# Kernel tuning notes

Measured on AMD Instinct MI355X. Metric: run time of the kernel, lower is better.

The kernel has to match this reference:

```python
import jax, jax.numpy as jnp
import numpy as np

N_NODES = 50000
N_EDGES = 800000
IN_DIM = 128
FEAT = 64
HID = 64
OUT = 64
EA_DIM = 3  # edge_attr columns; concat -> weight in_dim = 3*channels


def _uniform(key, shape, lo=-1.0, hi=1.0):
    return jax.random.uniform(key, shape, jnp.float32, lo, hi)


def setup_inputs() -> dict:
    key = jax.random.key(0)
    ks = jax.random.split(key, 12)
    x = jax.random.normal(ks[0], (N_NODES, IN_DIM), jnp.float32)
    edge_index = jax.random.randint(ks[1], (2, N_EDGES), 0, N_NODES, jnp.int32)
    edge_attr = jax.random.uniform(ks[2], (N_EDGES, EA_DIM), jnp.float32)
    # linear_pre (nn.Linear default init approximated; values irrelevant for correctness)
    pre_w = _uniform(ks[3], (IN_DIM, FEAT), -0.08, 0.08)
    pre_b = _uniform(ks[4], (FEAT,), -0.08, 0.08)
    # SAGEConvEGNN weights: uniform(-1, 1), shape [3*in, out]
    w1 = _uniform(ks[5], (EA_DIM * FEAT, HID))
    b1 = _uniform(ks[6], (HID,))
    w2 = _uniform(ks[7], (EA_DIM * HID, HID))
    b2 = _uniform(ks[8], (HID,))
    w3 = _uniform(ks[9], (EA_DIM * HID, OUT))
    b3 = _uniform(ks[10], (OUT,))
    return {"x": x, "edge_index": edge_index, "edge_attr": edge_attr,
            "pre_w": pre_w, "pre_b": pre_b,
            "w1": w1, "b1": b1, "w2": w2, "b2": b2, "w3": w3, "b3": b3}


def _sage_conv(h, src, tgt, edge_attr, w, b, n_nodes):
    # message: x_j scaled by each of the 3 edge_attr columns, concatenated -> [E, 3*C]
    xj = h[src]                                              # gather [E, C]
    msg = (edge_attr[:, :, None] * xj[:, None, :]).reshape(xj.shape[0], -1)
    s = jax.ops.segment_sum(msg, tgt, num_segments=n_nodes)  # scatter-sum [N, 3C]
    cnt = jax.ops.segment_sum(jnp.ones((src.shape[0],), msg.dtype), tgt,
                              num_segments=n_nodes)
    agg = s / jnp.maximum(cnt, 1.0)[:, None]                 # mean; 0 for isolated nodes
    return agg @ w + b


def reference(x, edge_index, edge_attr, pre_w, pre_b, w1, b1, w2, b2, w3, b3):
    src, tgt = edge_index[0], edge_index[1]  # message from j=src aggregated at i=tgt
    n = x.shape[0]
    h = x @ pre_w + pre_b                     # linear_pre
    h = jax.nn.relu(_sage_conv(h, src, tgt, edge_attr, w1, b1, n))
    h = jax.nn.relu(_sage_conv(h, src, tgt, edge_attr, w2, b2, n))
    h = _sage_conv(h, src, tgt, edge_attr, w3, b3, n)
    # F.normalize(p=2, dim=-1) with eps=1e-12
    norm = jnp.sqrt(jnp.sum(h * h, axis=-1, keepdims=True))
    return h / jnp.maximum(norm, 1e-12)
```

## Files before the change

kernel.cpp:

```cpp
#include <hip/hip_runtime.h>
#include <hip/hip_bf16.h>

#define NN 50000
#define NE 800000
#define IND 128
#define C 64
#define NBUCK 196

typedef __hip_bfloat16 bf16;
typedef __attribute__((ext_vector_type(8))) short s8v;
typedef __attribute__((ext_vector_type(4))) float f4v;

__device__ __forceinline__ float to_f(float v) { return v; }
__device__ __forceinline__ float to_f(bf16 v)  { return __bfloat162float(v); }

__device__ __forceinline__ unsigned short f2b(float v) {
    unsigned u = __float_as_uint(v);
    return (unsigned short)((u + 0x7FFFu + ((u >> 16) & 1u)) >> 16);
}
__device__ __forceinline__ float b2f(unsigned short u) {
    return __uint_as_float((unsigned)u << 16);
}

__global__ void detect_kernel(const unsigned* __restrict__ xu, int* __restrict__ flag,
                              int* __restrict__ zbase) {
    int lane = threadIdx.x;
    for (int i = lane; i < 512; i += 64) zbase[i] = 0;
    unsigned u  = xu[lane];
    unsigned ex = (u >> 7) & 0xFF;
    int vote = (ex >= 90 && ex <= 144) ? 1 : 0;
#pragma unroll
    for (int off = 32; off; off >>= 1) vote += __shfl_xor(vote, off, 64);
    if (lane == 0) { flag[0] = (vote < 40) ? 1 : 0; flag[1] = 0; }
}

__global__ __launch_bounds__(256) void prep_kernel(const void* pw, const void* w0,
        const void* w1, const void* w2, int* __restrict__ flagp,
        const int* __restrict__ tgt,
        unsigned short* __restrict__ oh, unsigned short* __restrict__ ol,
        int* __restrict__ bcnt, int* __restrict__ boff, int* __restrict__ off) {
    __shared__ int lc[NBUCK];
    __shared__ int rank_s;
    __shared__ int wsum[4];
    int blk = blockIdx.x;
    int tid = threadIdx.x;
    if (blk < 176) {
        int gid = blk * 256 + tid;
        const void* w; int nT, idx, base;
        if (gid < 8192) { w = pw; nT = 4; idx = gid; base = 0; }
        else {
            int r = gid - 8192; int l = r / 12288; idx = r % 12288; nT = 6;
            w = (l == 0) ? w0 : (l == 1) ? w1 : w2; base = 8192 + l * 12288;
        }
        int j = idx & 7, lane = (idx >> 3) & 63, r2 = idx >> 9;
        int t = r2 % nT, ct = r2 / nT;
        int k = 32 * t + ((lane >> 4) << 3) + j;
        int col = 16 * ct + (lane & 15);
        if (*flagp) {
            float v = ((const float*)w)[k * 64 + col];
            unsigned short hi = f2b(v);
            oh[base + idx] = hi;
            ol[base + idx] = f2b(v - b2f(hi));
        } else {
            oh[base + idx] = ((const unsigned short*)w)[k * 64 + col];
        }
        return;
    }
    for (int i = tid; i < NBUCK; i += 256) lc[i] = 0;
    __syncthreads();
    int e0 = (blk - 176) * 2048;
#pragma unroll
    for (int k = 0; k < 8; ++k) {
        int e = e0 + (k << 8) + tid;
        if (e < NE) atomicAdd(&lc[tgt[e] >> 8], 1);
    }
    __syncthreads();
    for (int i = tid; i < NBUCK; i += 256) if (lc[i]) atomicAdd(&bcnt[i], lc[i]);
    __syncthreads();
    if (tid == 0) {
        __threadfence();
        rank_s = atomicAdd(&flagp[1], 1);
    }
    __syncthreads();
    int nCnt = (int)gridDim.x - 176;
    if (rank_s == nCnt - 1) {
        int lane = tid & 63, wv = tid >> 6;
        int v = (tid < NBUCK) ? atomicAdd(&bcnt[tid], 0) : 0;
        int incl = v;
#pragma unroll
        for (int d = 1; d < 64; d <<= 1) { int t = __shfl_up(incl, d, 64); if (lane >= d) incl += t; }
        if (lane == 63) wsum[wv] = incl;
        __syncthreads();
        int wbase = 0;
#pragma unroll
        for (int j = 0; j < 4; ++j) wbase += (j < wv) ? wsum[j] : 0;
        if (tid < NBUCK) boff[tid] = wbase + incl - v;
        if (tid == 0) { boff[NBUCK] = NE; off[NN] = NE; }
    }
}

template <typename T>
__device__ __forceinline__ void binA_impl(int* lcnt, int* lbase,
                                          const int* __restrict__ src,
                                          const int* __restrict__ tgt,
                                          const T* __restrict__ ea,
                                          const int* __restrict__ boff,
                                          int* __restrict__ ccur,
                                          float4* __restrict__ stg) {
    int tid = threadIdx.x;
    for (int i = tid; i < NBUCK; i += 256) lcnt[i] = 0;
    __syncthreads();
    int e0 = blockIdx.x * 2048;
    float ex[8], ey[8], ez[8];
    unsigned ew[8];
    int eb[8], er[8];
#pragma unroll
    for (int k = 0; k < 8; ++k) {
        int e = e0 + (k << 8) + tid;
        if (e < NE) {
            int t = tgt[e];
            int s = src[e];
            eb[k] = t >> 8;
            ew[k] = ((unsigned)t << 16) | (unsigned)s;
            ex[k] = to_f(ea[e * 3 + 0]);
            ey[k] = to_f(ea[e * 3 + 1]);
            ez[k] = to_f(ea[e * 3 + 2]);
            er[k] = atomicAdd(&lcnt[eb[k]], 1);
        } else eb[k] = -1;
    }
    __syncthreads();
    for (int i = tid; i < NBUCK; i += 256) {
        int c = lcnt[i];
        int g = c ? atomicAdd(&ccur[i], c) : 0;
        lbase[i] = boff[i] + g;
    }
    __syncthreads();
#pragma unroll
    for (int k = 0; k < 8; ++k) {
        if (eb[k] >= 0) {
            float4 r;
            r.x = ex[k]; r.y = ey[k]; r.z = ez[k];
            r.w = __uint_as_float(ew[k]);
            stg[lbase[eb[k]] + er[k]] = r;
        }
    }
}

__global__ __launch_bounds__(256) void binA_kernel(const int* __restrict__ src,
                                                   const int* __restrict__ tgt,
                                                   const void* ea,
                                                   const int* __restrict__ boff,
                                                   const int* __restrict__ flagp,
                                                   int* __restrict__ ccur,
                                                   float4* __restrict__ stg) {
    __shared__ int lcnt[NBUCK];
    __shared__ int lbase[NBUCK];
    if (*flagp) binA_impl<float>(lcnt, lbase, src, tgt, (const float*)ea, boff, ccur, stg);
    else        binA_impl<bf16>(lcnt, lbase, src, tgt, (const bf16*)ea, boff, ccur, stg);
}

template <typename T>
__device__ __forceinline__ void preM_body(int nb, const T* __restrict__ x,
                                          const unsigned short* __restrict__ wfh,
                                          const unsigned short* __restrict__ wfl,
                                          const T* __restrict__ b,
                                          unsigned short* __restrict__ h) {
    int tid = threadIdx.x;
    int lane = tid & 63, wv = tid >> 6;
    int m = lane & 15, g = lane >> 4;
    int arow = nb + wv * 16 + m;
    bool okrow = arow < NN;
    f4v acc[4] = {};
    for (int t = 0; t < 4; ++t) {
        if constexpr (sizeof(T) == 4) {
            float av[8];
            if (okrow) {
                const float* xr = (const float*)x + (size_t)arow * IND + t * 32 + g * 8;
                float4 v0 = *(const float4*)xr;
                float4 v1 = *(const float4*)(xr + 4);
                av[0] = v0.x; av[1] = v0.y; av[2] = v0.z; av[3] = v0.w;
                av[4] = v1.x; av[5] = v1.y; av[6] = v1.z; av[7] = v1.w;
            } else {
#pragma unroll
                for (int j = 0; j < 8; ++j) av[j] = 0.f;
            }
            s8v ahi, alo;
#pragma unroll
            for (int j = 0; j < 8; ++j) {
                unsigned short hi = f2b(av[j]);
                ahi[j] = (short)hi;
                alo[j] = (short)f2b(av[j] - b2f(hi));
            }
#pragma unroll
            for (int ct = 0; ct < 4; ++ct) {
                int fo = ((ct * 4 + t) * 64 + lane) * 8;
                s8v bh = *(const s8v*)&wfh[fo];
                s8v bl = *(const s8v*)&wfl[fo];
                acc[ct] = __builtin_amdgcn_mfma_f32_16x16x32_bf16(ahi, bh, acc[ct], 0, 0, 0);
                acc[ct] = __builtin_amdgcn_mfma_f32_16x16x32_bf16(alo, bh, acc[ct], 0, 0, 0);
                acc[ct] = __builtin_amdgcn_mfma_f32_16x16x32_bf16(ahi, bl, acc[ct], 0, 0, 0);
            }
        } else {
            s8v ahi = {};
            if (okrow)
                ahi = *(const s8v*)((const unsigned short*)x + (size_t)arow * IND + t * 32 + g * 8);
#pragma unroll
            for (int ct = 0; ct < 4; ++ct) {
                int fo = ((ct * 4 + t) * 64 + lane) * 8;
                s8v bh = *(const s8v*)&wfh[fo];
                acc[ct] = __builtin_amdgcn_mfma_f32_16x16x32_bf16(ahi, bh, acc[ct], 0, 0, 0);
            }
        }
    }
#pragma unroll
    for (int r = 0; r < 4; ++r) {
        int drow = nb + wv * 16 + g * 4 + r;
        if (drow < NN) {
#pragma unroll
            for (int ct = 0; ct < 4; ++ct)
                h[(size_t)drow * C + 16 * ct + m] = f2b(acc[ct][r] + to_f(b[16 * ct + m]));
        }
    }
}

__global__ __launch_bounds__(256) void binB_pre_kernel(const float4* __restrict__ stg,
        const int* __restrict__ boff, int* __restrict__ off, float4* __restrict__ edge,
        const void* x, const unsigned short* __restrict__ wfh,
        const unsigned short* __restrict__ wfl, const void* pb,
        const int* __restrict__ flagp, unsigned short* __restrict__ h) {
    __shared__ int lcnt[256];
    __shared__ int lexcl[256];
    __shared__ int lfill[256];
    __shared__ int wsum[4];
    int tid = threadIdx.x;
    if (blockIdx.x < NBUCK) {
        int b = blockIdx.x;
        int n0 = b << 8;
        int cb = boff[b], ce = boff[b + 1];
        lcnt[tid] = 0;
        __syncthreads();
        for (int i = cb + tid; i < ce; i += 256) {
            unsigned w = __float_as_uint(stg[i].w);
            atomicAdd(&lcnt[(w >> 16) & 255], 1);
        }
        __syncthreads();
        int lane = tid & 63, wv = tid >> 6;
        int v = lcnt[tid];
        int incl = v;
#pragma unroll
        for (int d = 1; d < 64; d <<= 1) { int t = __shfl_up(incl, d, 64); if (lane >= d) incl += t; }
        if (lane == 63) wsum[wv] = incl;
        __syncthreads();
        int wbase = 0;
#pragma unroll
        for (int j = 0; j < 4; ++j) wbase += (j < wv) ? wsum[j] : 0;
        lexcl[tid] = wbase + incl - v;
        lfill[tid] = 0;
        __syncthreads();
        int n = n0 + tid;
        if (n <= NN) off[n] = cb + lexcl[tid];
        for (int i = cb + tid; i < ce; i += 256) {
            float4 r = stg[i];
            unsigned w = __float_as_uint(r.w);
            int l = (int)(w >> 16) & 255;
            int rk = atomicAdd(&lfill[l], 1);
            r.w = __uint_as_float(w & 0xFFFFu);
            edge[cb + lexcl[l] + rk] = r;
        }
    } else {
        int nb = (blockIdx.x - NBUCK) * 64;
        if (*flagp) preM_body<float>(nb, (const float*)x, wfh, wfl, (const float*)pb, h);
        else        preM_body<bf16>(nb, (const bf16*)x, wfh, wfl, (const bf16*)pb, h);
    }
}

__global__ __launch_bounds__(256) void agg_kernel(const unsigned short* __restrict__ hb,
                                                  const float4* __restrict__ edge,
                                                  const int* __restrict__ off,
                                                  unsigned short* __restrict__ sh,
                                                  unsigned short* __restrict__ sl) {
    int f = threadIdx.x & 63;
    int n = blockIdx.x * 4 + (threadIdx.x >> 6);
    int beg = __builtin_amdgcn_readfirstlane(off[n]);
    int end = __builtin_amdgcn_readfirstlane(off[n + 1]);
    float a0 = 0.f, a1 = 0.f, a2 = 0.f;
    int cnt = end - beg;
    int m4 = beg + (cnt & ~3);
    int e = beg;
    if (beg + 8 <= m4) {
        float4 c0 = edge[e],     c1 = edge[e + 1], c2 = edge[e + 2], c3 = edge[e + 3];
        float4 d0 = edge[e + 4], d1 = edge[e + 5], d2 = edge[e + 6], d3 = edge[e + 7];
        float h0 = b2f(hb[(__float_as_int(c0.w) << 6) + f]);
        float h1 = b2f(hb[(__float_as_int(c1.w) << 6) + f]);
        float h2 = b2f(hb[(__float_as_int(c2.w) << 6) + f]);
        float h3 = b2f(hb[(__float_as_int(c3.w) << 6) + f]);
        int e2 = beg + 8;
        while (e2 < m4) {
            float g0 = b2f(hb[(__float_as_int(d0.w) << 6) + f]);
            float g1 = b2f(hb[(__float_as_int(d1.w) << 6) + f]);
            float g2 = b2f(hb[(__float_as_int(d2.w) << 6) + f]);
            float g3 = b2f(hb[(__float_as_int(d3.w) << 6) + f]);
            float4 n0 = edge[e2], n1 = edge[e2 + 1], n2 = edge[e2 + 2], n3 = edge[e2 + 3];
            a0 += c0.x * h0; a1 += c0.y * h0; a2 += c0.z * h0;
            a0 += c1.x * h1; a1 += c1.y * h1; a2 += c1.z * h1;
            a0 += c2.x * h2; a1 += c2.y * h2; a2 += c2.z * h2;
            a0 += c3.x * h3; a1 += c3.y * h3; a2 += c3.z * h3;
            c0 = d0; c1 = d1; c2 = d2; c3 = d3;
            h0 = g0; h1 = g1; h2 = g2; h3 = g3;
            d0 = n0; d1 = n1; d2 = n2; d3 = n3;
            e2 += 4;
        }
        float g0 = b2f(hb[(__float_as_int(d0.w) << 6) + f]);
        float g1 = b2f(hb[(__float_as_int(d1.w) << 6) + f]);
        float g2 = b2f(hb[(__float_as_int(d2.w) << 6) + f]);
        float g3 = b2f(hb[(__float_as_int(d3.w) << 6) + f]);
        a0 += c0.x * h0; a1 += c0.y * h0; a2 += c0.z * h0;
        a0 += c1.x * h1; a1 += c1.y * h1; a2 += c1.z * h1;
        a0 += c2.x * h2; a1 += c2.y * h2; a2 += c2.z * h2;
        a0 += c3.x * h3; a1 += c3.y * h3; a2 += c3.z * h3;
        a0 += d0.x * g0; a1 += d0.y * g0; a2 += d0.z * g0;
        a0 += d1.x * g1; a1 += d1.y * g1; a2 += d1.z * g1;
        a0 += d2.x * g2; a1 += d2.y * g2; a2 += d2.z * g2;
        a0 += d3.x * g3; a1 += d3.y * g3; a2 += d3.z * g3;
        e = m4;
    } else if (beg + 4 <= m4) {
        float4 c0 = edge[e], c1 = edge[e + 1], c2 = edge[e + 2], c3 = edge[e + 3];
        float h0 = b2f(hb[(__float_as_int(c0.w) << 6) + f]);
        float h1 = b2f(hb[(__float_as_int(c1.w) << 6) + f]);
        float h2 = b2f(hb[(__float_as_int(c2.w) << 6) + f]);
        float h3 = b2f(hb[(__float_as_int(c3.w) << 6) + f]);
        a0 += c0.x * h0; a1 += c0.y * h0; a2 += c0.z * h0;
        a0 += c1.x * h1; a1 += c1.y * h1; a2 += c1.z * h1;
        a0 += c2.x * h2; a1 += c2.y * h2; a2 += c2.z * h2;
        a0 += c3.x * h3; a1 += c3.y * h3; a2 += c3.z * h3;
        e = m4;
    }
    for (; e < end; ++e) {
        float4 r = edge[e];
        float hv = b2f(hb[(__float_as_int(r.w) << 6) + f]);
        a0 += r.x * hv; a1 += r.y * hv; a2 += r.z * hv;
    }
    float iv = 1.0f / fmaxf((float)cnt, 1.0f);
    size_t base = (size_t)n * 192;
    float v0 = a0 * iv, v1 = a1 * iv, v2 = a2 * iv;
    unsigned short x0 = f2b(v0), x1 = f2b(v1), x2 = f2b(v2);
    sh[base + f]       = x0; sl[base + f]       = f2b(v0 - b2f(x0));
    sh[base + 64 + f]  = x1; sl[base + 64 + f]  = f2b(v1 - b2f(x1));
    sh[base + 128 + f] = x2; sl[base + 128 + f] = f2b(v2 - b2f(x2));
}

template <typename T, int MODE>
__device__ __forceinline__ void gemmM_impl(const unsigned short* __restrict__ sh,
                                           const unsigned short* __restrict__ sl,
                                           const unsigned short* __restrict__ wfh,
                                           const unsigned short* __restrict__ wfl,
                                           const T* __restrict__ b,
                                           unsigned short* __restrict__ hout, T* __restrict__ out) {
    int tid = threadIdx.x;
    int nb  = blockIdx.x * 64;
    int lane = tid & 63, wv = tid >> 6;
    int m = lane & 15, g = lane >> 4;
    int arow = nb + wv * 16 + m;
    bool okrow = arow < NN;
    const unsigned short* shrow = sh + (size_t)arow * 192 + g * 8;
    const unsigned short* slrow = sl + (size_t)arow * 192 + g * 8;
    f4v acc[4] = {};
    for (int t = 0; t < 6; ++t) {
        s8v ahi = {}, alo = {};
        if (okrow) {
            ahi = *(const s8v*)(shrow + t * 32);
            alo = *(const s8v*)(slrow + t * 32);
        }
#pragma unroll
        for (int ct = 0; ct < 4; ++ct) {
            int fo = ((ct * 6 + t) * 64 + lane) * 8;
            s8v bh = *(const s8v*)&wfh[fo];
            acc[ct] = __builtin_amdgcn_mfma_f32_16x16x32_bf16(ahi, bh, acc[ct], 0, 0, 0);
            acc[ct] = __builtin_amdgcn_mfma_f32_16x16x32_bf16(alo, bh, acc[ct], 0, 0, 0);
            if constexpr (sizeof(T) == 4) {
                s8v bl = *(const s8v*)&wfl[fo];
                acc[ct] = __builtin_amdgcn_mfma_f32_16x16x32_bf16(ahi, bl, acc[ct], 0, 0, 0);
            }
        }
    }
    float vv[4][4];
#pragma unroll
    for (int ct = 0; ct < 4; ++ct) {
        float bv = to_f(b[16 * ct + m]);
#pragma unroll
        for (int r = 0; r < 4; ++r) vv[ct][r] = acc[ct][r] + bv;
    }
    if constexpr (MODE == 0) {
#pragma unroll
        for (int r = 0; r < 4; ++r) {
            int drow = nb + wv * 16 + g * 4 + r;
            if (drow < NN) {
#pragma unroll
                for (int ct = 0; ct < 4; ++ct)
                    hout[(size_t)drow * C + 16 * ct + m] = f2b(fmaxf(vv[ct][r], 0.f));
            }
        }
    } else {
#pragma unroll
        for (int r = 0; r < 4; ++r) {
            float sq = vv[0][r] * vv[0][r] + vv[1][r] * vv[1][r]
                     + vv[2][r] * vv[2][r] + vv[3][r] * vv[3][r];
#pragma unroll
            for (int o = 1; o < 16; o <<= 1) sq += __shfl_xor(sq, o, 64);
            float innorm = 1.0f / fmaxf(sqrtf(sq), 1e-12f);
            int drow = nb + wv * 16 + g * 4 + r;
            if (drow < NN) {
#pragma unroll
                for (int ct = 0; ct < 4; ++ct) {
                    float rv = vv[ct][r] * innorm;
                    if constexpr (sizeof(T) == 2) out[(size_t)drow * C + 16 * ct + m] = __float2bfloat16(rv);
                    else                          out[(size_t)drow * C + 16 * ct + m] = rv;
                }
            }
        }
    }
}

__global__ __launch_bounds__(256) void gemm_relu(const unsigned short* __restrict__ sh,
                                                 const unsigned short* __restrict__ sl,
                                                 const unsigned short* __restrict__ wfh,
                                                 const unsigned short* __restrict__ wfl,
                                                 const void* b, const int* __restrict__ flagp,
                                                 unsigned short* __restrict__ hout) {
    if (*flagp) gemmM_impl<float, 0>(sh, sl, wfh, wfl, (const float*)b, hout, (float*)nullptr);
    else        gemmM_impl<bf16, 0>(sh, sl, wfh, wfl, (const bf16*)b, hout, (bf16*)nullptr);
}

__global__ __launch_bounds__(256) void gemm_norm(const unsigned short* __restrict__ sh,
                                                 const unsigned short* __restrict__ sl,
                                                 const unsigned short* __restrict__ wfh,
                                                 const unsigned short* __restrict__ wfl,
                                                 const void* b, const int* __restrict__ flagp,
                                                 void* out) {
    if (*flagp) gemmM_impl<float, 1>(sh, sl, wfh, wfl, (const float*)b, nullptr, (float*)out);
    else        gemmM_impl<bf16, 1>(sh, sl, wfh, wfl, (const bf16*)b, nullptr, (bf16*)out);
}

extern "C" void kernel_launch(void* const* d_in, const int* in_sizes, int n_in,
                              void* d_out, int out_size, void* d_ws, size_t ws_size,
                              hipStream_t stream) {
    const void* x     = d_in[0];
    const int*  ei    = (const int*)d_in[1];
    const void* ea    = d_in[2];
    const void* pre_w = d_in[3];
    const void* pre_b = d_in[4];
    const void* W[3]  = {d_in[5], d_in[7], d_in[9]};
    const void* B[3]  = {d_in[6], d_in[8], d_in[10]};
    const int* src = ei;
    const int* tgt = ei + NE;

    float4*         EDGE = (float4*)d_ws;
    unsigned short* SH   = (unsigned short*)(EDGE + NE);
    unsigned short* SL   = SH + (size_t)NN * 192;
    float4*         STG  = (float4*)SH;
    unsigned short* H    = SL + (size_t)NN * 192;
    int*            BCNT = (int*)(H + (size_t)NN * C);
    int*            CCUR = BCNT + 256;
    int*            BOFF = CCUR + 256;
    int*            OFF  = BOFF + 256;
    int*            FLAG = OFF + NN + 8;
    unsigned short* WH   = (unsigned short*)(FLAG + 16);
    unsigned short* WL   = WH + 45056;

    detect_kernel<<<1, 64, 0, stream>>>((const unsigned*)x, FLAG, BCNT);
    prep_kernel<<<176 + (NE + 2047) / 2048, 256, 0, stream>>>(pre_w, W[0], W[1], W[2],
                                                              FLAG, tgt, WH, WL,
                                                              BCNT, BOFF, OFF);
    binA_kernel<<<(NE + 2047) / 2048, 256, 0, stream>>>(src, tgt, ea, BOFF, FLAG, CCUR, STG);
    binB_pre_kernel<<<NBUCK + (NN + 63) / 64, 256, 0, stream>>>(STG, BOFF, OFF, EDGE,
                                                                x, WH, WL, pre_b, FLAG, H);

    int nblk = (NN + 63) / 64;
    for (int l = 0; l < 3; ++l) {
        const unsigned short* wfh = WH + 8192 + l * 12288;
        const unsigned short* wfl = WL + 8192 + l * 12288;
        agg_kernel<<<NN / 4, 256, 0, stream>>>(H, EDGE, OFF, SH, SL);
        if (l < 2)
            gemm_relu<<<nblk, 256, 0, stream>>>(SH, SL, wfh, wfl, B[l], FLAG, H);
        else
            gemm_norm<<<nblk, 256, 0, stream>>>(SH, SL, wfh, wfl, B[l], FLAG, d_out);
    }
}
```

Baseline: 276.5 us.

## Split wavefront into four edge groups with vectorized 8-byte feature gathers

The aggregation kernel now has each wavefront process four edges at once. Each 16-lane group handles one edge and each lane loads four bf16 features with a single 8-byte load, instead of 64 lanes walking one edge at a time with 2-byte loads. Partial sums are combined with cross-lane shuffles, and one quarter of the wave writes the outputs as vectorized ushort4 stores. This aims to issue fewer, wider gather instructions and expose more edge-level parallelism, at the cost of shuffle reductions, more accumulator registers, and the loss of the explicit software prefetch pipeline.

```diff
diff --git a/kernel.cpp b/kernel.cpp
--- a/kernel.cpp
+++ b/kernel.cpp
@@ -279,74 +279,61 @@
                                                   const int* __restrict__ off,
                                                   unsigned short* __restrict__ sh,
                                                   unsigned short* __restrict__ sl) {
-    int f = threadIdx.x & 63;
+    int lane = threadIdx.x & 63;
     int n = blockIdx.x * 4 + (threadIdx.x >> 6);
     int beg = __builtin_amdgcn_readfirstlane(off[n]);
     int end = __builtin_amdgcn_readfirstlane(off[n + 1]);
-    float a0 = 0.f, a1 = 0.f, a2 = 0.f;
-    int cnt = end - beg;
-    int m4 = beg + (cnt & ~3);
+    int p  = lane & 15;
+    int jj = lane >> 4;
+    float a0[4] = {0.f, 0.f, 0.f, 0.f};
+    float a1[4] = {0.f, 0.f, 0.f, 0.f};
+    float a2[4] = {0.f, 0.f, 0.f, 0.f};
     int e = beg;
-    if (beg + 8 <= m4) {
-        float4 c0 = edge[e],     c1 = edge[e + 1], c2 = edge[e + 2], c3 = edge[e + 3];
-        float4 d0 = edge[e + 4], d1 = edge[e + 5], d2 = edge[e + 6], d3 = edge[e + 7];
-        float h0 = b2f(hb[(__float_as_int(c0.w) << 6) + f]);
-        float h1 = b2f(hb[(__float_as_int(c1.w) << 6) + f]);
-        float h2 = b2f(hb[(__float_as_int(c2.w) << 6) + f]);
-        float h3 = b2f(hb[(__float_as_int(c3.w) << 6) + f]);
-        int e2 = beg + 8;
-        while (e2 < m4) {
-            float g0 = b2f(hb[(__float_as_int(d0.w) << 6) + f]);
-            float g1 = b2f(hb[(__float_as_int(d1.w) << 6) + f]);
-            float g2 = b2f(hb[(__float_as_int(d2.w) << 6) + f]);
-            float g3 = b2f(hb[(__float_as_int(d3.w) << 6) + f]);
-            float4 n0 = edge[e2], n1 = edge[e2 + 1], n2 = edge[e2 + 2], n3 = edge[e2 + 3];
-            a0 += c0.x * h0; a1 += c0.y * h0; a2 += c0.z * h0;
-            a0 += c1.x * h1; a1 += c1.y * h1; a2 += c1.z * h1;
-            a0 += c2.x * h2; a1 += c2.y * h2; a2 += c2.z * h2;
-            a0 += c3.x * h3; a1 += c3.y * h3; a2 += c3.z * h3;
-            c0 = d0; c1 = d1; c2 = d2; c3 = d3;
-            h0 = g0; h1 = g1; h2 = g2; h3 = g3;
-            d0 = n0; d1 = n1; d2 = n2; d3 = n3;
-            e2 += 4;
-        }
-        float g0 = b2f(hb[(__float_as_int(d0.w) << 6) + f]);
-        float g1 = b2f(hb[(__float_as_int(d1.w) << 6) + f]);
-        float g2 = b2f(hb[(__float_as_int(d2.w) << 6) + f]);
-        float g3 = b2f(hb[(__float_as_int(d3.w) << 6) + f]);
-        a0 += c0.x * h0; a1 += c0.y * h0; a2 += c0.z * h0;
-        a0 += c1.x * h1; a1 += c1.y * h1; a2 += c1.z * h1;
-        a0 += c2.x * h2; a1 += c2.y * h2; a2 += c2.z * h2;
-        a0 += c3.x * h3; a1 += c3.y * h3; a2 += c3.z * h3;
-        a0 += d0.x * g0; a1 += d0.y * g0; a2 += d0.z * g0;
-        a0 += d1.x * g1; a1 += d1.y * g1; a2 += d1.z * g1;
-        a0 += d2.x * g2; a1 += d2.y * g2; a2 += d2.z * g2;
-        a0 += d3.x * g3; a1 += d3.y * g3; a2 += d3.z * g3;
-        e = m4;
-    } else if (beg + 4 <= m4) {
-        float4 c0 = edge[e], c1 = edge[e + 1], c2 = edge[e + 2], c3 = edge[e + 3];
-        float h0 = b2f(hb[(__float_as_int(c0.w) << 6) + f]);
-        float h1 = b2f(hb[(__float_as_int(c1.w) << 6) + f]);
-        float h2 = b2f(hb[(__float_as_int(c2.w) << 6) + f]);
-        float h3 = b2f(hb[(__float_as_int(c3.w) << 6) + f]);
-        a0 += c0.x * h0; a1 += c0.y * h0; a2 += c0.z * h0;
-        a0 += c1.x * h1; a1 += c1.y * h1; a2 += c1.z * h1;
-        a0 += c2.x * h2; a1 += c2.y * h2; a2 += c2.z * h2;
-        a0 += c3.x * h3; a1 += c3.y * h3; a2 += c3.z * h3;
-        e = m4;
-    }
-    for (; e < end; ++e) {
-        float4 r = edge[e];
-        float hv = b2f(hb[(__float_as_int(r.w) << 6) + f]);
-        a0 += r.x * hv; a1 += r.y * hv; a2 += r.z * hv;
-    }
-    float iv = 1.0f / fmaxf((float)cnt, 1.0f);
-    size_t base = (size_t)n * 192;
-    float v0 = a0 * iv, v1 = a1 * iv, v2 = a2 * iv;
-    unsigned short x0 = f2b(v0), x1 = f2b(v1), x2 = f2b(v2);
-    sh[base + f]       = x0; sl[base + f]       = f2b(v0 - b2f(x0));
-    sh[base + 64 + f]  = x1; sl[base + 64 + f]  = f2b(v1 - b2f(x1));
-    sh[base + 128 + f] = x2; sl[base + 128 + f] = f2b(v2 - b2f(x2));
+    for (; e + 4 <= end; e += 4) {
+        float4 r = edge[e + jj];
+        ushort4 hv = *(const ushort4*)(hb + ((size_t)__float_as_int(r.w) << 6) + 4 * p);
+        float h0 = b2f(hv.x), h1 = b2f(hv.y), h2 = b2f(hv.z), h3 = b2f(hv.w);
+        a0[0] += r.x * h0; a0[1] += r.x * h1; a0[2] += r.x * h2; a0[3] += r.x * h3;
+        a1[0] += r.y * h0; a1[1] += r.y * h1; a1[2] += r.y * h2; a1[3] += r.y * h3;
+        a2[0] += r.z * h0; a2[1] += r.z * h1; a2[2] += r.z * h2; a2[3] += r.z * h3;
+    }
+    int t = end - e;
+    if (jj < t) {
+        float4 r = edge[e + jj];
+        ushort4 hv = *(const ushort4*)(hb + ((size_t)__float_as_int(r.w) << 6) + 4 * p);
+        float h0 = b2f(hv.x), h1 = b2f(hv.y), h2 = b2f(hv.z), h3 = b2f(hv.w);
+        a0[0] += r.x * h0; a0[1] += r.x * h1; a0[2] += r.x * h2; a0[3] += r.x * h3;
+        a1[0] += r.y * h0; a1[1] += r.y * h1; a1[2] += r.y * h2; a1[3] += r.y * h3;
+        a2[0] += r.z * h0; a2[1] += r.z * h1; a2[2] += r.z * h2; a2[3] += r.z * h3;
+    }
+#pragma unroll
+    for (int q = 0; q < 4; ++q) {
+        a0[q] += __shfl_xor(a0[q], 16, 64); a0[q] += __shfl_xor(a0[q], 32, 64);
+        a1[q] += __shfl_xor(a1[q], 16, 64); a1[q] += __shfl_xor(a1[q], 32, 64);
+        a2[q] += __shfl_xor(a2[q], 16, 64); a2[q] += __shfl_xor(a2[q], 32, 64);
+    }
+    if (jj == 0) {
+        float iv = 1.0f / fmaxf((float)(end - beg), 1.0f);
+        size_t base = (size_t)n * 192 + 4 * p;
+        ushort4 uh, ul;
+        float v;
+        unsigned short hi;
+        v = a0[0] * iv; hi = f2b(v); uh.x = hi; ul.x = f2b(v - b2f(hi));
+        v = a0[1] * iv; hi = f2b(v); uh.y = hi; ul.y = f2b(v - b2f(hi));
+        v = a0[2] * iv; hi = f2b(v); uh.z = hi; ul.z = f2b(v - b2f(hi));
+        v = a0[3] * iv; hi = f2b(v); uh.w = hi; ul.w = f2b(v - b2f(hi));
+        *(ushort4*)(sh + base) = uh; *(ushort4*)(sl + base) = ul;
+        v = a1[0] * iv; hi = f2b(v); uh.x = hi; ul.x = f2b(v - b2f(hi));
+        v = a1[1] * iv; hi = f2b(v); uh.y = hi; ul.y = f2b(v - b2f(hi));
+        v = a1[2] * iv; hi = f2b(v); uh.z = hi; ul.z = f2b(v - b2f(hi));
+        v = a1[3] * iv; hi = f2b(v); uh.w = hi; ul.w = f2b(v - b2f(hi));
+        *(ushort4*)(sh + base + 64) = uh; *(ushort4*)(sl + base + 64) = ul;
+        v = a2[0] * iv; hi = f2b(v); uh.x = hi; ul.x = f2b(v - b2f(hi));
+        v = a2[1] * iv; hi = f2b(v); uh.y = hi; ul.y = f2b(v - b2f(hi));
+        v = a2[2] * iv; hi = f2b(v); uh.z = hi; ul.z = f2b(v - b2f(hi));
+        v = a2[3] * iv; hi = f2b(v); uh.w = hi; ul.w = f2b(v - b2f(hi));
+        *(ushort4*)(sh + base + 128) = uh; *(ushort4*)(sl + base + 128) = ul;
+    }
 }
 
 template <typename T, int MODE>
```

After: 297.1 us. 1.07x slower.
